# Kernel tuning notes

Hardware: AMD Instinct MI355X
Metric: run time of the kernel (lower is better)

Reference implementation:

```python
import jax, jax.numpy as jnp
import numpy as np

OUT_SIZE = 7      # roi_layer out_size
SAMPLE_NUM = 2    # roi_layer sample_num
STRIDES = (4, 8, 16, 32)
IMG = 1024.0


def _roi_align(feat_nchw, rois, out, scale, sn):
    """mmdet RoIAlign (aligned=False), vectorized over all rois.

    feat_nchw: [B, C, H, W]; rois: [N, 5] = (batch_idx, x1, y1, x2, y2).
    Returns [N, C, out, out].
    """
    feat = jnp.transpose(feat_nchw, (0, 2, 3, 1))  # [B, H, W, C]
    B, H, W, C = feat.shape
    N = rois.shape[0]
    b = rois[:, 0].astype(jnp.int32)
    x1 = rois[:, 1] * scale
    y1 = rois[:, 2] * scale
    x2 = rois[:, 3] * scale
    y2 = rois[:, 4] * scale
    roi_w = jnp.maximum(x2 - x1, 1.0)
    roi_h = jnp.maximum(y2 - y1, 1.0)
    # sample-point offsets within the roi, in bin units: [out*sn]
    grid = (jnp.arange(out, dtype=jnp.float32)[:, None]
            + (jnp.arange(sn, dtype=jnp.float32)[None, :] + 0.5) / sn).reshape(-1)
    ys = y1[:, None] + grid[None, :] * (roi_h / out)[:, None]  # [N, S]
    xs = x1[:, None] + grid[None, :] * (roi_w / out)[:, None]  # [N, S]

    def interp1(coord, size):
        valid = ((coord > -1.0) & (coord < size)).astype(coord.dtype)
        c = jnp.clip(coord, 0.0, size - 1.0)
        lo = jnp.floor(c).astype(jnp.int32)
        hi = jnp.minimum(lo + 1, size - 1)
        w_hi = c - lo.astype(coord.dtype)
        w_lo = 1.0 - w_hi
        # zero-out out-of-image samples via the weights
        return lo, hi, w_lo * valid, w_hi * valid

    y_lo, y_hi, wy_lo, wy_hi = interp1(ys, H)
    x_lo, x_hi, wx_lo, wx_hi = interp1(xs, W)

    def gather(yi, xi):
        # [N, S, S, C]
        return feat[b[:, None, None], yi[:, :, None], xi[:, None, :]]

    val = (gather(y_lo, x_lo) * (wy_lo[:, :, None] * wx_lo[:, None, :])[..., None]
           + gather(y_lo, x_hi) * (wy_lo[:, :, None] * wx_hi[:, None, :])[..., None]
           + gather(y_hi, x_lo) * (wy_hi[:, :, None] * wx_lo[:, None, :])[..., None]
           + gather(y_hi, x_hi) * (wy_hi[:, :, None] * wx_hi[:, None, :])[..., None])
    # average the sn x sn samples inside each bin
    val = val.reshape(N, out, sn, out, sn, C).mean(axis=(2, 4))  # [N, out, out, C]
    return jnp.transpose(val, (0, 3, 1, 2))  # [N, C, out, out]


def setup_inputs() -> dict:
    key = jax.random.key(0)
    ks = jax.random.split(key, 8)
    feats = {}
    for i, hw in enumerate([256, 128, 64, 32]):
        feats[f"feat{i}"] = jax.random.normal(ks[i], (1, 256, hw, hw), dtype=jnp.float32)
    N = 1000
    u = jax.random.uniform(ks[4], (N, 4), dtype=jnp.float32)
    x1 = u[:, 0] * (IMG - 64.0)
    y1 = u[:, 1] * (IMG - 64.0)
    w = 16.0 + u[:, 2] * 480.0
    h = 16.0 + u[:, 3] * 480.0
    x2 = jnp.minimum(x1 + w, IMG - 1.0)
    y2 = jnp.minimum(y1 + h, IMG - 1.0)
    bidx = jnp.zeros((N,), dtype=jnp.float32)
    rois = jnp.stack([bidx, x1, y1, x2, y2], axis=1)
    feats["rois"] = rois
    return feats


def reference(feat0, feat1, feat2, feat3, rois):
    feats = (feat0, feat1, feat2, feat3)
    # PASingleRoIExtractor multi-level path: RoIAlign every roi on every level,
    # then elementwise max across levels.
    out = _roi_align(feats[0], rois, OUT_SIZE, 1.0 / STRIDES[0], SAMPLE_NUM)
    for lvl in range(1, len(feats)):
        out = jnp.maximum(out, _roi_align(feats[lvl], rois, OUT_SIZE,
                                          1.0 / STRIDES[lvl], SAMPLE_NUM))
    return out
```

## Files before the change

### kernel.cpp

```cpp
#include <hip/hip_runtime.h>


#define NCH 256
#define NBIN 49

typedef _Float16 half2v __attribute__((ext_vector_type(2)));

#if defined(__has_builtin)
#if __has_builtin(__builtin_amdgcn_fdot2)
#define HAVE_FDOT2 1
#endif
#if __has_builtin(__builtin_amdgcn_cvt_pkrtz)
#define HAVE_PKRTZ 1
#endif
#endif

__device__ __constant__ int    d_H[4]      = {256, 128, 64, 32};
__device__ __constant__ float  d_scale[4]  = {0.25f, 0.125f, 0.0625f, 0.03125f};
__device__ __constant__ int    d_off4[4]   = {0, 2097152, 2621440, 2752512};
__device__ __constant__ size_t d_offu[4]   = {0, 16777216, 20971520, 22020096};
__device__ __constant__ int    d_tstart[4] = {0, 4096, 5120, 5376};
__device__ __constant__ int    d_tilesx[4] = {4, 2, 1, 1};

__device__ __forceinline__ int pack_h2(float a, float b) {
#ifdef HAVE_PKRTZ
    return __builtin_bit_cast(int, __builtin_amdgcn_cvt_pkrtz(a, b));
#else
    half2v h;
    h.x = (_Float16)a;
    h.y = (_Float16)b;
    return __builtin_bit_cast(int, h);
#endif
}
__device__ __forceinline__ half2v bc_h2(int x) { return __builtin_bit_cast(half2v, x); }
__device__ __forceinline__ half2v bc_h2u(unsigned x) { return __builtin_bit_cast(half2v, x); }

#ifdef HAVE_FDOT2
#define ACC2(uLLc, uLHc, w2, k0)                                                                       \
    acc[k0] = __builtin_amdgcn_fdot2(bc_h2u(__builtin_amdgcn_perm((uLHc), (uLLc), 0x05040100u)), (w2), \
                                     acc[k0], false);                                                  \
    acc[k0 + 1] = __builtin_amdgcn_fdot2(                                                              \
        bc_h2u(__builtin_amdgcn_perm((uLHc), (uLLc), 0x07060302u)), (w2), acc[k0 + 1], false)
#else
#define ACC2(uLLc, uLHc, w2, k0)                                       \
    do {                                                               \
        half2v a_ = bc_h2u(uLLc), b_ = bc_h2u(uLHc);                   \
        float w0_ = (float)(w2).x, w1_ = (float)(w2).y;                \
        acc[k0]     = fmaf((float)a_.x, w0_, acc[k0]);                 \
        acc[k0]     = fmaf((float)b_.x, w1_, acc[k0]);                 \
        acc[k0 + 1] = fmaf((float)a_.y, w0_, acc[k0 + 1]);             \
        acc[k0 + 1] = fmaf((float)b_.y, w1_, acc[k0 + 1]);             \
    } while (0)
#endif

__device__ __forceinline__ void do_sample(const uint4* __restrict__ base, float* acc, int4 ye,
                                          int4 xe) {
    uint4 uLL = base[ye.x + xe.x];
    uint4 uLH = base[ye.x + xe.y];
    uint4 uHL = base[ye.y + xe.x];
    uint4 uHH = base[ye.y + xe.y];
    half2v wx = bc_h2(xe.z);
    half2v wlo = bc_h2(ye.z) * wx;
    half2v whi = bc_h2(ye.w) * wx;
    ACC2(uLL.x, uLH.x, wlo, 0);
    ACC2(uLL.y, uLH.y, wlo, 2);
    ACC2(uLL.z, uLH.z, wlo, 4);
    ACC2(uLL.w, uLH.w, wlo, 6);
    ACC2(uHL.x, uHH.x, whi, 0);
    ACC2(uHL.y, uHH.y, whi, 2);
    ACC2(uHL.z, uHH.z, whi, 4);
    ACC2(uHL.w, uHH.w, whi, 6);
}

__global__ __launch_bounds__(256) void transpose_fused(
    const float* __restrict__ f0, const float* __restrict__ f1, const float* __restrict__ f2,
    const float* __restrict__ f3, unsigned short* __restrict__ out) {
    __shared__ float tile[64 * 66];

    const int bid = blockIdx.x;
    const int lvl = (bid >= d_tstart[1]) + (bid >= d_tstart[2]) + (bid >= d_tstart[3]);
    int rem = bid - d_tstart[lvl];
    const int H = d_H[lvl];
    const int tnx = d_tilesx[lvl];
    const int xt = rem % tnx;
    rem /= tnx;
    const int y = rem % H;
    const int cg = rem / H;
    const int x0 = xt * 64;
    const float* in = (lvl == 0) ? f0 : (lvl == 1) ? f1 : (lvl == 2) ? f2 : f3;
    unsigned short* o = out + d_offu[lvl];

    const int tid = threadIdx.x;
    const int tx2 = tid & 31;
    const int wv = tid >> 5;
    const size_t HW = (size_t)H * H;
    const float* inp = in + (size_t)(cg * 64) * HW + (size_t)y * H + x0;
    const bool xin = (x0 + tx2 * 2) < H;
#pragma unroll
    for (int r = 0; r < 8; ++r) {
        int cl = wv * 8 + r;
        float2 v = make_float2(0.0f, 0.0f);
        if (xin) v = *(const float2*)(inp + (size_t)cl * HW + tx2 * 2);
        *(float2*)&tile[cl * 66 + tx2 * 2] = v;
    }
    __syncthreads();

    const int o8 = tid & 7;
    const int xi = tid >> 3;
#pragma unroll
    for (int pass = 0; pass < 2; ++pass) {
        int px = xi + pass * 32;
        int x = x0 + px;
        if (x < H) {
            const float* col = &tile[o8 * 8 * 66 + px];
            unsigned d0 = (unsigned)pack_h2(col[0 * 66], col[1 * 66]);
            unsigned d1 = (unsigned)pack_h2(col[2 * 66], col[3 * 66]);
            unsigned d2 = (unsigned)pack_h2(col[4 * 66], col[5 * 66]);
            unsigned d3 = (unsigned)pack_h2(col[6 * 66], col[7 * 66]);
            uint4* dst = (uint4*)(o + (size_t)(y * H + x) * NCH + cg * 64 + o8 * 8);
            *dst = make_uint4(d0, d1, d2, d3);
        }
    }
}

__global__ __launch_bounds__(256) void roi_main4(const uint4* __restrict__ ws,
                                                 const float* __restrict__ rois,
                                                 float* __restrict__ out) {
    __shared__ float smem[64 * NBIN];
    __shared__ int4 tbl[4][2][14];

    const int n = blockIdx.x >> 2;
    const int quarter = blockIdx.x & 3;
    const int tid = threadIdx.x;
    const float* r = rois + (size_t)n * 5;

    if (tid < 112) {
        int lvl = tid / 28;
        int e = tid % 28;
        int axis = e / 14;
        int s = e % 14;
        int H = d_H[lvl];
        float sc = d_scale[lvl];
        float a = (axis ? r[1] : r[2]) * sc;
        float b2 = (axis ? r[3] : r[4]) * sc;
        float binsz = fmaxf(b2 - a, 1.0f) * (1.0f / 7.0f);
        float g = (float)(s >> 1) + 0.25f + 0.5f * (float)(s & 1);
        float coord = a + g * binsz;
        float valid = (coord > -1.0f && coord < (float)H) ? 1.0f : 0.0f;
        float c = fminf(fmaxf(coord, 0.0f), (float)H - 1.0f);
        int lo = (int)floorf(c);
        int hi = min(lo + 1, H - 1);
        float whi = (c - (float)lo) * valid;
        float wlo = (1.0f - (c - (float)lo)) * valid;
        int mult = axis ? 32 : H * 32;
        int4 t;
        t.x = lo * mult;
        t.y = hi * mult;
        if (axis) {
            t.z = pack_h2(wlo, whi);
            t.w = 0;
        } else {
            t.z = pack_h2(wlo, wlo);
            t.w = pack_h2(whi, whi);
        }
        tbl[lvl][axis][s] = t;
    }
    __syncthreads();

    const int p = tid & 7;
    const int h = tid >> 3;
    const int octet = quarter * 8 + p;
    const int bstart = (h * NBIN) >> 5;
    const int bend = ((h + 1) * NBIN) >> 5;

    for (int b = bstart; b < bend; ++b) {
        int by = b / 7;
        int bx = b - by * 7;
        float m[8];
#pragma unroll
        for (int k = 0; k < 8; ++k) m[k] = -3.402823e38f;
#pragma unroll
        for (int lvl = 0; lvl < 4; ++lvl) {
            const uint4* base = ws + d_off4[lvl] + octet;
            int4 ye0 = tbl[lvl][0][2 * by];
            int4 ye1 = tbl[lvl][0][2 * by + 1];
            int4 xe0 = tbl[lvl][1][2 * bx];
            int4 xe1 = tbl[lvl][1][2 * bx + 1];
            float acc[8];
#pragma unroll
            for (int k = 0; k < 8; ++k) acc[k] = 0.0f;
            do_sample(base, acc, ye0, xe0);
            do_sample(base, acc, ye0, xe1);
            do_sample(base, acc, ye1, xe0);
            do_sample(base, acc, ye1, xe1);
#pragma unroll
            for (int k = 0; k < 8; ++k) m[k] = fmaxf(m[k], acc[k] * 0.25f);
        }
#pragma unroll
        for (int k = 0; k < 8; ++k) smem[(p * 8 + k) * NBIN + b] = m[k];
    }
    __syncthreads();

    float4* o4 = (float4*)(out + (size_t)n * (NCH * NBIN) + (size_t)quarter * (64 * NBIN));
    const float4* s4 = (const float4*)smem;
    for (int i = tid; i < 64 * NBIN / 4; i += 256) o4[i] = s4[i];
}

__device__ __forceinline__ int4 make_entry_f(float coord, int size, int mult) {
    float valid = (coord > -1.0f && coord < (float)size) ? 1.0f : 0.0f;
    float c = fminf(fmaxf(coord, 0.0f), (float)size - 1.0f);
    int lo = (int)floorf(c);
    int hi = min(lo + 1, size - 1);
    float whi = (c - (float)lo) * valid;
    float wlo = (1.0f - (c - (float)lo)) * valid;
    int4 r;
    r.x = lo * mult;
    r.y = hi * mult;
    r.z = __float_as_int(wlo);
    r.w = __float_as_int(whi);
    return r;
}

__global__ __launch_bounds__(256) void roi_direct(
    const float* __restrict__ f0, const float* __restrict__ f1, const float* __restrict__ f2,
    const float* __restrict__ f3, const float* __restrict__ rois, float* __restrict__ out) {
    const int n = blockIdx.x;
    const int c = threadIdx.x;
    const float* feats[4] = {f0, f1, f2, f3};
    const float* r = rois + (size_t)n * 5;
    for (int b = 0; b < NBIN; ++b) {
        int by = b / 7;
        int bx = b - by * 7;
        float m = -3.402823e38f;
#pragma unroll
        for (int lvl = 0; lvl < 4; ++lvl) {
            int H = d_H[lvl];
            float sc = d_scale[lvl];
            float x1 = r[1] * sc, y1 = r[2] * sc, x2 = r[3] * sc, y2 = r[4] * sc;
            float bw = fmaxf(x2 - x1, 1.0f) * (1.0f / 7.0f);
            float bh = fmaxf(y2 - y1, 1.0f) * (1.0f / 7.0f);
            const float* f = feats[lvl] + (size_t)c * H * H;
            float acc = 0.0f;
#pragma unroll
            for (int sy = 0; sy < 2; ++sy) {
#pragma unroll
                for (int sx = 0; sx < 2; ++sx) {
                    float yc = y1 + ((float)by + 0.25f + 0.5f * sy) * bh;
                    float xc = x1 + ((float)bx + 0.25f + 0.5f * sx) * bw;
                    int4 ey = make_entry_f(yc, H, H);
                    int4 ex = make_entry_f(xc, H, 1);
                    float wyl = __int_as_float(ey.z), wyh = __int_as_float(ey.w);
                    float wxl = __int_as_float(ex.z), wxh = __int_as_float(ex.w);
                    acc += f[ey.x + ex.x] * wyl * wxl + f[ey.x + ex.y] * wyl * wxh +
                           f[ey.y + ex.x] * wyh * wxl + f[ey.y + ex.y] * wyh * wxh;
                }
            }
            m = fmaxf(m, acc * 0.25f);
        }
        out[((size_t)n * NCH + c) * NBIN + b] = m;
    }
}

extern "C" void kernel_launch(void* const* d_in, const int* in_sizes, int n_in, void* d_out,
                              int out_size, void* d_ws, size_t ws_size, hipStream_t stream) {
    const float* f0 = (const float*)d_in[0];
    const float* f1 = (const float*)d_in[1];
    const float* f2 = (const float*)d_in[2];
    const float* f3 = (const float*)d_in[3];
    const float* rois = (const float*)d_in[4];
    const int nrois = in_sizes[4] / 5;
    float* out = (float*)d_out;

    const size_t need = 44564480;
    if (ws_size >= need) {
        unsigned short* ws = (unsigned short*)d_ws;
        transpose_fused<<<5504, 256, 0, stream>>>(f0, f1, f2, f3, ws);
        roi_main4<<<4 * nrois, 256, 0, stream>>>((const uint4*)d_ws, rois, out);
    } else {
        roi_direct<<<nrois, 256, 0, stream>>>(f0, f1, f2, f3, rois, out);
    }
}
```

Before: 217.0 us.

## Fuse transpose and RoI kernels into persistent cooperative kernel with grid sync

Merges the layout-transpose kernel and the RoI-align kernel into one persistent cooperative kernel. Blocks grid-stride over transpose tiles, wait on a grid-wide barrier, then grid-stride over RoI work. The aim is to remove the second launch and the gap at the kernel boundary. It also changes the shared-memory transpose tile to a column-major, padding-65 layout and replaces div/mod with shifts. The risks are grid-sync cost, reduced occupancy from the persistent grid, and host-side occupancy queries on every call.

```diff
diff --git a/kernel.cpp b/kernel.cpp
--- a/kernel.cpp
+++ b/kernel.cpp
@@ -1,8 +1,12 @@
 #include <hip/hip_runtime.h>
+#include <hip/hip_cooperative_groups.h>
+
+namespace cg = cooperative_groups;
 
 
 #define NCH 256
 #define NBIN 49
+#define NTILE 5504
 
 typedef _Float16 half2v __attribute__((ext_vector_type(2)));
 
@@ -21,6 +25,8 @@
 __device__ __constant__ size_t d_offu[4]   = {0, 16777216, 20971520, 22020096};
 __device__ __constant__ int    d_tstart[4] = {0, 4096, 5120, 5376};
 __device__ __constant__ int    d_tilesx[4] = {4, 2, 1, 1};
+__device__ __constant__ int    d_tshift[4] = {2, 1, 0, 0};
+__device__ __constant__ int    d_hshift[4] = {8, 7, 6, 5};
 
 __device__ __forceinline__ int pack_h2(float a, float b) {
 #ifdef HAVE_PKRTZ
@@ -72,66 +78,60 @@
     ACC2(uHL.w, uHH.w, whi, 6);
 }
 
-__global__ __launch_bounds__(256) void transpose_fused(
-    const float* __restrict__ f0, const float* __restrict__ f1, const float* __restrict__ f2,
-    const float* __restrict__ f3, unsigned short* __restrict__ out) {
-    __shared__ float tile[64 * 66];
-
-    const int bid = blockIdx.x;
-    const int lvl = (bid >= d_tstart[1]) + (bid >= d_tstart[2]) + (bid >= d_tstart[3]);
-    int rem = bid - d_tstart[lvl];
+__device__ __forceinline__ void transpose_tile(int t, const float* __restrict__ f0,
+                                               const float* __restrict__ f1,
+                                               const float* __restrict__ f2,
+                                               const float* __restrict__ f3,
+                                               unsigned short* __restrict__ out, float* tile,
+                                               int tid) {
+    const int lvl = (t >= d_tstart[1]) + (t >= d_tstart[2]) + (t >= d_tstart[3]);
+    int rem = t - d_tstart[lvl];
     const int H = d_H[lvl];
-    const int tnx = d_tilesx[lvl];
-    const int xt = rem % tnx;
-    rem /= tnx;
-    const int y = rem % H;
-    const int cg = rem / H;
+    const int xt = rem & (d_tilesx[lvl] - 1);
+    rem >>= d_tshift[lvl];
+    const int y = rem & (H - 1);
+    const int cgi = rem >> d_hshift[lvl];
     const int x0 = xt * 64;
     const float* in = (lvl == 0) ? f0 : (lvl == 1) ? f1 : (lvl == 2) ? f2 : f3;
     unsigned short* o = out + d_offu[lvl];
 
-    const int tid = threadIdx.x;
-    const int tx2 = tid & 31;
-    const int wv = tid >> 5;
+    const int tx2 = tid & 31, wv = tid >> 5;
     const size_t HW = (size_t)H * H;
-    const float* inp = in + (size_t)(cg * 64) * HW + (size_t)y * H + x0;
-    const bool xin = (x0 + tx2 * 2) < H;
+    const float* inp = in + (size_t)(cgi * 64) * HW + (size_t)y * H + x0;
+    const bool xin = (x0 + 2 * tx2) < H;
 #pragma unroll
     for (int r = 0; r < 8; ++r) {
         int cl = wv * 8 + r;
         float2 v = make_float2(0.0f, 0.0f);
-        if (xin) v = *(const float2*)(inp + (size_t)cl * HW + tx2 * 2);
-        *(float2*)&tile[cl * 66 + tx2 * 2] = v;
+        if (xin) v = *(const float2*)(inp + (size_t)cl * HW + 2 * tx2);
+        tile[(2 * tx2) * 65 + cl] = v.x;
+        tile[(2 * tx2 + 1) * 65 + cl] = v.y;
     }
     __syncthreads();
-
-    const int o8 = tid & 7;
-    const int xi = tid >> 3;
+    const int o8 = tid & 7, xi = tid >> 3;
 #pragma unroll
     for (int pass = 0; pass < 2; ++pass) {
         int px = xi + pass * 32;
         int x = x0 + px;
         if (x < H) {
-            const float* col = &tile[o8 * 8 * 66 + px];
-            unsigned d0 = (unsigned)pack_h2(col[0 * 66], col[1 * 66]);
-            unsigned d1 = (unsigned)pack_h2(col[2 * 66], col[3 * 66]);
-            unsigned d2 = (unsigned)pack_h2(col[4 * 66], col[5 * 66]);
-            unsigned d3 = (unsigned)pack_h2(col[6 * 66], col[7 * 66]);
-            uint4* dst = (uint4*)(o + (size_t)(y * H + x) * NCH + cg * 64 + o8 * 8);
-            *dst = make_uint4(d0, d1, d2, d3);
+            const float* col = &tile[px * 65 + o8 * 8];
+            unsigned d0 = (unsigned)pack_h2(col[0], col[1]);
+            unsigned d1 = (unsigned)pack_h2(col[2], col[3]);
+            unsigned d2 = (unsigned)pack_h2(col[4], col[5]);
+            unsigned d3 = (unsigned)pack_h2(col[6], col[7]);
+            *(uint4*)(o + (size_t)(y * H + x) * NCH + cgi * 64 + o8 * 8) =
+                make_uint4(d0, d1, d2, d3);
         }
     }
-}
-
-__global__ __launch_bounds__(256) void roi_main4(const uint4* __restrict__ ws,
-                                                 const float* __restrict__ rois,
-                                                 float* __restrict__ out) {
-    __shared__ float smem[64 * NBIN];
-    __shared__ int4 tbl[4][2][14];
-
-    const int n = blockIdx.x >> 2;
-    const int quarter = blockIdx.x & 3;
-    const int tid = threadIdx.x;
+    __syncthreads();
+}
+
+__device__ __forceinline__ void roi_block(int vb, const uint4* __restrict__ ws,
+                                          const float* __restrict__ rois,
+                                          float* __restrict__ out, float* smem, int4* tbl,
+                                          int tid) {
+    const int n = vb >> 2;
+    const int quarter = vb & 3;
     const float* r = rois + (size_t)n * 5;
 
     if (tid < 112) {
@@ -153,17 +153,17 @@
         float whi = (c - (float)lo) * valid;
         float wlo = (1.0f - (c - (float)lo)) * valid;
         int mult = axis ? 32 : H * 32;
-        int4 t;
-        t.x = lo * mult;
-        t.y = hi * mult;
+        int4 tt;
+        tt.x = lo * mult;
+        tt.y = hi * mult;
         if (axis) {
-            t.z = pack_h2(wlo, whi);
-            t.w = 0;
+            tt.z = pack_h2(wlo, whi);
+            tt.w = 0;
         } else {
-            t.z = pack_h2(wlo, wlo);
-            t.w = pack_h2(whi, whi);
+            tt.z = pack_h2(wlo, wlo);
+            tt.w = pack_h2(whi, whi);
         }
-        tbl[lvl][axis][s] = t;
+        tbl[tid] = tt;
     }
     __syncthreads();
 
@@ -182,10 +182,10 @@
 #pragma unroll
         for (int lvl = 0; lvl < 4; ++lvl) {
             const uint4* base = ws + d_off4[lvl] + octet;
-            int4 ye0 = tbl[lvl][0][2 * by];
-            int4 ye1 = tbl[lvl][0][2 * by + 1];
-            int4 xe0 = tbl[lvl][1][2 * bx];
-            int4 xe1 = tbl[lvl][1][2 * bx + 1];
+            int4 ye0 = tbl[lvl * 28 + 2 * by];
+            int4 ye1 = tbl[lvl * 28 + 2 * by + 1];
+            int4 xe0 = tbl[lvl * 28 + 14 + 2 * bx];
+            int4 xe1 = tbl[lvl * 28 + 14 + 2 * bx + 1];
             float acc[8];
 #pragma unroll
             for (int k = 0; k < 8; ++k) acc[k] = 0.0f;
@@ -204,6 +204,52 @@
     float4* o4 = (float4*)(out + (size_t)n * (NCH * NBIN) + (size_t)quarter * (64 * NBIN));
     const float4* s4 = (const float4*)smem;
     for (int i = tid; i < 64 * NBIN / 4; i += 256) o4[i] = s4[i];
+}
+
+__global__ __launch_bounds__(256, 8) void roi_mega(
+    const float* __restrict__ f0, const float* __restrict__ f1, const float* __restrict__ f2,
+    const float* __restrict__ f3, const float* __restrict__ rois, float* __restrict__ out,
+    unsigned short* __restrict__ wsp, int nrois) {
+    __shared__ float sh[64 * 65];
+    const int tid = threadIdx.x;
+    const int G = gridDim.x;
+
+    for (int t = blockIdx.x; t < NTILE; t += G)
+        transpose_tile(t, f0, f1, f2, f3, wsp, sh, tid);
+
+    cg::this_grid().sync();
+
+    const uint4* ws4 = (const uint4*)wsp;
+    float* smem = sh;
+    int4* tbl = (int4*)(sh + 64 * NBIN);
+    const int nvb = 4 * nrois;
+    for (int vb = blockIdx.x; vb < nvb; vb += G) {
+        __syncthreads();
+        roi_block(vb, ws4, rois, out, smem, tbl, tid);
+    }
+}
+
+__global__ __launch_bounds__(256, 8) void transpose_k(
+    const float* __restrict__ f0, const float* __restrict__ f1, const float* __restrict__ f2,
+    const float* __restrict__ f3, unsigned short* __restrict__ wsp) {
+    __shared__ float sh[64 * 65];
+    const int tid = threadIdx.x;
+    for (int t = blockIdx.x; t < NTILE; t += gridDim.x)
+        transpose_tile(t, f0, f1, f2, f3, wsp, sh, tid);
+}
+
+__global__ __launch_bounds__(256, 8) void roi_k(const uint4* __restrict__ ws,
+                                                const float* __restrict__ rois,
+                                                float* __restrict__ out, int nrois) {
+    __shared__ float sh[64 * 65];
+    const int tid = threadIdx.x;
+    float* smem = sh;
+    int4* tbl = (int4*)(sh + 64 * NBIN);
+    const int nvb = 4 * nrois;
+    for (int vb = blockIdx.x; vb < nvb; vb += gridDim.x) {
+        __syncthreads();
+        roi_block(vb, ws, rois, out, smem, tbl, tid);
+    }
 }
 
 __device__ __forceinline__ int4 make_entry_f(float coord, int size, int mult) {
@@ -268,15 +314,29 @@
     const float* f2 = (const float*)d_in[2];
     const float* f3 = (const float*)d_in[3];
     const float* rois = (const float*)d_in[4];
-    const int nrois = in_sizes[4] / 5;
+    int nrois = in_sizes[4] / 5;
     float* out = (float*)d_out;
 
     const size_t need = 44564480;
-    if (ws_size >= need) {
-        unsigned short* ws = (unsigned short*)d_ws;
-        transpose_fused<<<5504, 256, 0, stream>>>(f0, f1, f2, f3, ws);
-        roi_main4<<<4 * nrois, 256, 0, stream>>>((const uint4*)d_ws, rois, out);
-    } else {
+    if (ws_size < need) {
         roi_direct<<<nrois, 256, 0, stream>>>(f0, f1, f2, f3, rois, out);
-    }
-}
+        return;
+    }
+    unsigned short* wsp = (unsigned short*)d_ws;
+
+    int bpc = 0;
+    hipError_t e1 = hipOccupancyMaxActiveBlocksPerMultiprocessor(&bpc, roi_mega, 256, 0);
+    int dev = 0, ncu = 0;
+    hipGetDevice(&dev);
+    hipError_t e2 = hipDeviceGetAttribute(&ncu, hipDeviceAttributeMultiprocessorCount, dev);
+    if (e1 == hipSuccess && e2 == hipSuccess && bpc > 0 && ncu > 0) {
+        int grid = bpc * ncu;
+        if (grid > 4096) grid = 4096;
+        void* args[] = {(void*)&f0, (void*)&f1, (void*)&f2, (void*)&f3,
+                        (void*)&rois, (void*)&out, (void*)&wsp, (void*)&nrois};
+        hipError_t le = hipLaunchCooperativeKernel(roi_mega, dim3(grid), dim3(256), args, 0, stream);
+        if (le == hipSuccess) return;
+    }
+    transpose_k<<<NTILE, 256, 0, stream>>>(f0, f1, f2, f3, wsp);
+    roi_k<<<4 * nrois, 256, 0, stream>>>((const uint4*)d_ws, rois, out, nrois);
+}
```

Measured after the change: 388.2 us. +78.9%, slower.
